# Kernel optimization log

Measured on AMD Instinct MI355X. Metric: run time of the kernel, lower is better.

## Reference

```python
import jax, jax.numpy as jnp
import numpy as np
from jax import lax

V_JOINTS = 25
N_SCALES = 13
C1 = 96
N_SEG = 50
EPS = 1e-5

# NTU RGB+D 25-joint skeleton edges (0-indexed)
_EDGES = [(0,1),(1,20),(2,20),(3,2),(4,20),(5,4),(6,5),(7,6),(8,20),(9,8),
          (10,9),(11,10),(12,0),(13,12),(14,13),(15,14),(16,0),(17,16),
          (18,17),(19,18),(21,22),(22,7),(23,24),(24,11)]


def _build_A_powers():
    # MS-G3D disentangled multi-scale adjacency: k-hop shells, D^-1/2 A D^-1/2 normalized
    A = np.zeros((V_JOINTS, V_JOINTS), dtype=np.float64)
    for i, j in _EDGES:
        A[i, j] = 1.0
        A[j, i] = 1.0
    I = np.eye(V_JOINTS)
    mats = []
    for k in range(N_SCALES):
        if k == 0:
            Ak = I.copy()
        else:
            Ak = (np.minimum(np.linalg.matrix_power(A + I, k), 1)
                  - np.minimum(np.linalg.matrix_power(A + I, k - 1), 1))
            Ak = Ak + I  # with_self=True
        d = Ak.sum(-1)
        Dinv = np.diag(d ** -0.5)
        mats.append(Dinv @ Ak @ Dinv)
    return np.concatenate(mats, axis=0).astype(np.float32)  # (13*25, 25)


def _segments(T, n_seg):
    # Segment boundaries exactly as the torch code: int(round(linspace(1, T, n_seg+1)))
    t_vec = [int(round(v)) for v in np.linspace(1, T, n_seg + 1)]
    lens = [t_vec[i + 1] - t_vec[i] for i in range(n_seg)]
    L = max(lens)
    idx = np.zeros((n_seg, L), dtype=np.int32)
    mask = np.zeros((n_seg, L), dtype=np.float32)
    for s in range(n_seg):
        start = t_vec[s] - 1
        for l in range(L):
            idx[s, l] = min(start + l, T - 2)
            mask[s, l] = 1.0 if l < lens[s] else 0.0
    sp_idx = np.array([t - 1 for t in t_vec[:-1]], dtype=np.int32)
    return idx, mask, sp_idx


def setup_inputs() -> dict:
    key = jax.random.key(0)
    ks = jax.random.split(key, 18)
    N, M, C, T, V = 4, 2, 3, 300, V_JOINTS
    num_classes = 60
    Cbn = M * C * V                       # 150
    Dlog = C1 + C1 * (C1 - 1) // 2        # 4656 (depth-2 logsig dims)
    Din = C1 + Dlog                       # 4752 (start pos + logsig)
    f = lambda k, s: jax.random.normal(k, s, dtype=jnp.float32)
    return {
        'x': f(ks[0], (N, M, C, T, V)),
        'bn_g': 1.0 + 0.1 * f(ks[1], (Cbn,)),
        'bn_b': 0.1 * f(ks[2], (Cbn,)),
        'bn_m': 0.1 * f(ks[3], (Cbn,)),
        'bn_v': jax.random.uniform(ks[4], (Cbn,), minval=0.5, maxval=1.5),
        'A_powers': jnp.asarray(_build_A_powers()),
        'A_res': jax.random.uniform(ks[5], (N_SCALES * V, V), minval=-1e-6, maxval=1e-6),
        'W_gcn': f(ks[6], (C1, N_SCALES * C)) / np.sqrt(N_SCALES * C),
        'b_gcn': 0.1 * f(ks[7], (C1,)),
        'bn2_g': 1.0 + 0.1 * f(ks[8], (C1,)),
        'bn2_b': 0.1 * f(ks[9], (C1,)),
        'bn2_m': 0.1 * f(ks[10], (C1,)),
        'bn2_v': jax.random.uniform(ks[11], (C1,), minval=0.5, maxval=1.5),
        'W_ih': f(ks[12], (4 * C1, Din)) / np.sqrt(Din),
        'W_hh': f(ks[13], (4 * C1, C1)) / np.sqrt(C1),
        'b_ih': 0.1 * f(ks[14], (4 * C1,)),
        'b_hh': 0.1 * f(ks[15], (4 * C1,)),
        'W_fc': f(ks[16], (num_classes, C1)) / np.sqrt(C1),
        'b_fc': 0.1 * f(ks[17], (num_classes,)),
    }


def reference(x, bn_g, bn_b, bn_m, bn_v, A_powers, A_res, W_gcn, b_gcn,
              bn2_g, bn2_b, bn2_m, bn2_v, W_ih, W_hh, b_ih, b_hh, W_fc, b_fc):
    N, M, C, T, V = x.shape
    NM = N * M
    # --- data_bn (inference BatchNorm1d over M*V*C channels) ---
    xb = x.transpose(0, 1, 4, 2, 3).reshape(N, M * V * C, T)
    xb = (xb - bn_m[:, None]) * (bn_g / jnp.sqrt(bn_v + EPS))[:, None] + bn_b[:, None]
    xg = xb.reshape(NM, V, C, T).transpose(0, 2, 3, 1)          # (NM, C, T, V)
    # --- MS_GCN: multi-scale disentangled graph conv ---
    A = A_powers + A_res                                        # (S*V, V)
    sup = jnp.einsum('vu,nctu->nctv', A, xg)                    # (NM, C, T, S*V)
    sup = sup.reshape(NM, C, T, N_SCALES, V).transpose(0, 3, 1, 2, 4)
    sup = sup.reshape(NM, N_SCALES * C, T, V)
    y = jnp.einsum('oc,nctv->notv', W_gcn, sup) + b_gcn[None, :, None, None]
    y = (y - bn2_m[None, :, None, None]) * (bn2_g / jnp.sqrt(bn2_v + EPS))[None, :, None, None] \
        + bn2_b[None, :, None, None]
    y = jax.nn.relu(y)                                          # (NM, C1, T, V)
    # --- LogSigRNN: per-joint temporal path, depth-2 log-signature per segment ---
    p = y.transpose(0, 3, 2, 1).reshape(NM * V, T, C1)          # (B, T, C1)
    idx, mask, sp_idx = _segments(T, N_SEG)
    dx = jnp.diff(p, axis=1)                                    # (B, T-1, C1)
    dseg = dx[:, idx] * mask[None, :, :, None]                  # (B, nseg, L, C1)
    pseg = jnp.cumsum(dseg, axis=2) - dseg                      # exclusive prefix within segment
    s1 = dseg.sum(axis=2)                                       # level-1: total increment
    Q = jnp.einsum('bslc,bsld->bscd', pseg, dseg)               # (B, nseg, C1, C1)
    levy = 0.5 * (Q - jnp.swapaxes(Q, -1, -2))                  # level-2 (Levy area)
    iu, ju = np.triu_indices(C1, 1)
    ls2 = levy[:, :, iu, ju]                                    # (B, nseg, 4560)
    start_pos = p[:, sp_idx, :]                                 # (B, nseg, C1)
    feat = jnp.concatenate([start_pos, s1, ls2], axis=-1)       # (B, nseg, 4752)
    # --- LSTM (torch gate order i,f,g,o) ---
    B = feat.shape[0]
    xw = jnp.einsum('btd,gd->btg', feat, W_ih) + (b_ih + b_hh)
    def step(carry, xt):
        h, c = carry
        g = xt + h @ W_hh.T
        i, fg, gg, o = jnp.split(g, 4, axis=-1)
        c = jax.nn.sigmoid(fg) * c + jax.nn.sigmoid(i) * jnp.tanh(gg)
        h = jax.nn.sigmoid(o) * jnp.tanh(c)
        return (h, c), h
    h0 = jnp.zeros((B, C1), feat.dtype)
    _, hs = lax.scan(step, (h0, h0), jnp.swapaxes(xw, 0, 1))
    hs = jnp.swapaxes(hs, 0, 1)                                 # (B, nseg, C1)
    out = hs.reshape(NM, V, N_SEG, C1).transpose(0, 3, 2, 1)    # (NM, C1, nseg, V)
    out = out.reshape(N, M, C1, -1).mean(axis=3).mean(axis=1)   # (N, C1)
    return out @ W_fc.T + b_fc
```

## Files before the change

### kernel.cpp

```cpp
#include <hip/hip_runtime.h>
#include <math.h>

#define KF 4752
#define KP 4768
#define KSTEPS 149
#define G4 384
#define NPAIR 4560
#define EPSBN 1e-5f
#define XWHALF 3840000

typedef float f32x4 __attribute__((ext_vector_type(4)));
typedef short s16x8 __attribute__((ext_vector_type(8)));

__device__ __forceinline__ unsigned short f2bf(float x){
  unsigned u = __float_as_uint(x);
  return (unsigned short)((u + 0x7fffu + ((u>>16)&1u)) >> 16);
}
__device__ __forceinline__ float bf2f(unsigned short h){
  return __uint_as_float(((unsigned)h)<<16);
}

__device__ __forceinline__ int seg_start(int s){ return (s<=24)? 6*s : 149 + 6*(s-25); }
__device__ __forceinline__ int seg_len(int s){ return (s==24)?5:6; }

#define NB_GEFF 1407
#define NB_BEFF 1200
#define NB_PAIR 18
#define NB_WSPL 7152

__global__ __launch_bounds__(256) void kPre(
    const float* bn_g,const float* bn_b,const float* bn_m,const float* bn_v,
    const float* Ap,const float* Ar,const float* Wg,const float* bg,
    const float* bn2_g,const float* bn2_b,const float* bn2_m,const float* bn2_v,
    const float* wih,
    float* geffT, float* beffT, int* pairs, unsigned short* whi, unsigned short* wlo)
{
  int bid = blockIdx.x, tid = threadIdx.x;
  if (bid < NB_GEFF){
    int idx = bid*256 + tid;
    if (idx >= 2*96*25*75) return;
    int cu = idx % 75; int rest = idx/75;
    int v = rest % 25; rest /= 25;
    int o = rest % 96; int m = rest / 96;
    int c = cu/25, u = cu%25;
    int ch = (m*25+u)*3 + c;
    float s1 = bn_g[ch] / sqrtf(bn_v[ch] + EPSBN);
    float s2 = bn2_g[o] / sqrtf(bn2_v[o] + EPSBN);
    float acc = 0.f;
    for (int k=0;k<13;k++){
      float a = Ap[(k*25+v)*25+u] + Ar[(k*25+v)*25+u];
      acc += Wg[o*39 + k*3 + c] * a;
    }
    geffT[((size_t)(m*75+cu))*2400 + v*96 + o] = acc * s1 * s2;
  } else if (bid < NB_GEFF + NB_BEFF){
    int wid  = ((bid-NB_GEFF)*256 + tid) >> 6;
    int lane = tid & 63;
    if (wid >= 2*96*25) return;
    int v = wid % 25; int rest = wid/25; int o = rest % 96; int m = rest/96;
    float acc = 0.f;
    #pragma unroll
    for (int it=0; it<16; ++it){
      int item = it*64 + lane;
      if (item < 975){
        int k = item / 75; int cu = item % 75; int c = cu/25, u = cu%25;
        int ch = (m*25+u)*3 + c;
        float s1 = bn_g[ch] / sqrtf(bn_v[ch] + EPSBN);
        float t1 = bn_b[ch] - bn_m[ch]*s1;
        float a  = Ap[(k*25+v)*25+u] + Ar[(k*25+v)*25+u];
        acc += Wg[o*39 + k*3 + c] * a * t1;
      }
    }
    #pragma unroll
    for (int off=32; off; off>>=1) acc += __shfl_down(acc, off);
    if (lane == 0){
      acc += bg[o];
      float s2 = bn2_g[o]/sqrtf(bn2_v[o]+EPSBN);
      beffT[m*2400 + v*96 + o] = s2*(acc - bn2_m[o]) + bn2_b[o];
    }
  } else if (bid < NB_GEFF + NB_BEFF + NB_PAIR){
    int k = (bid - NB_GEFF - NB_BEFF)*256 + tid;
    if (k >= NPAIR) return;
    int i=0, rem=k;
    while (rem >= 95 - i){ rem -= (95 - i); i++; }
    int j = i + 1 + rem;
    pairs[k] = (i<<7) | j;
  } else {
    int idx = (bid - NB_GEFF - NB_BEFF - NB_PAIR)*256 + tid;
    if (idx >= G4*KP) return;
    int g = idx / KP, k = idx % KP;
    float v = (k < KF) ? wih[(size_t)g*KF + k] : 0.f;
    unsigned short h = f2bf(v);
    whi[idx] = h;
    wlo[idx] = f2bf(v - bf2f(h));
  }
}

#define TTILE 10
__global__ __launch_bounds__(256) void kP(const float* x, const float* geffT, const float* beffT, float* p){
  int nm = blockIdx.y;
  int t0 = blockIdx.x * TTILE;
  int m  = nm % 2;
  __shared__ float xs[75*TTILE];
  int tid = threadIdx.x;
  for (int li = tid; li < 75*TTILE; li += 256){
    int u = li % 25; int rest = li/25; int tt = rest % TTILE; int c = rest / TTILE;
    xs[(c*25+u)*TTILE + tt] = x[(((size_t)nm*3 + c)*300 + (t0+tt))*25 + u];
  }
  __syncthreads();
  const float* gT = geffT + (size_t)m*75*2400;
  for (int ow = tid; ow < 2400; ow += 256){
    int o = ow % 96, v = ow / 96;
    float b = beffT[m*2400 + ow];
    float acc[TTILE];
    #pragma unroll
    for (int t=0;t<TTILE;t++) acc[t] = b;
    for (int cu=0; cu<75; cu++){
      float gv = gT[(size_t)cu*2400 + ow];
      #pragma unroll
      for (int t=0;t<TTILE;t++) acc[t] += gv * xs[cu*TTILE+t];
    }
    #pragma unroll
    for (int t=0;t<TTILE;t++)
      p[((size_t)(nm*25+v)*300 + t0+t)*96 + o] = fmaxf(acc[t], 0.f);
  }
}

__global__ __launch_bounds__(256) void kFeat(const float* p, const int* pairs,
                                             unsigned short* fhi, unsigned short* flo, int row0){
  int row = row0 + blockIdx.x;
  int b = row / 50, s = row % 50;
  int S = seg_start(s), len = seg_len(s);
  __shared__ float ps8[96][12];
  __shared__ float ds8[96][12];
  int tid = threadIdx.x;
  size_t base = (size_t)blockIdx.x * KP;
  if (tid < 96){
    int c = tid;
    float pv[7];
    #pragma unroll
    for (int l=0;l<7;l++) pv[l] = p[((size_t)b*300 + S + l)*96 + c];
    float run = 0.f;
    #pragma unroll
    for (int l=0;l<6;l++){
      float d = (l < len) ? (pv[l+1]-pv[l]) : 0.f;
      ps8[c][l] = run; ds8[c][l] = d; run += d;
    }
    ps8[c][6] = 0.f; ps8[c][7] = 0.f; ds8[c][6] = 0.f; ds8[c][7] = 0.f;
    unsigned short h0 = f2bf(pv[0]);
    fhi[base + c] = h0; flo[base + c] = f2bf(pv[0] - bf2f(h0));
    unsigned short h1 = f2bf(run);
    fhi[base + 96 + c] = h1; flo[base + 96 + c] = f2bf(run - bf2f(h1));
  } else if (tid < 112){
    int c = KF + (tid - 96);
    fhi[base + c] = 0; flo[base + c] = 0;
  }
  __syncthreads();
  for (int g8 = tid; g8 < NPAIR/8; g8 += 256){
    int k0 = g8*8;
    s16x8 vh, vl;
    int icur = -1;
    f32x4 pi0={0,0,0,0}, pi1={0,0,0,0}, di0={0,0,0,0}, di1={0,0,0,0};
    #pragma unroll
    for (int e=0;e<8;e++){
      int pr = pairs[k0+e]; int i = pr>>7, j = pr&127;
      if (i != icur){
        icur = i;
        pi0 = *(const f32x4*)&ps8[i][0]; pi1 = *(const f32x4*)&ps8[i][4];
        di0 = *(const f32x4*)&ds8[i][0]; di1 = *(const f32x4*)&ds8[i][4];
      }
      f32x4 pj0 = *(const f32x4*)&ps8[j][0], pj1 = *(const f32x4*)&ps8[j][4];
      f32x4 dj0 = *(const f32x4*)&ds8[j][0], dj1 = *(const f32x4*)&ds8[j][4];
      float q = pi0.x*dj0.x + pi0.y*dj0.y + pi0.z*dj0.z + pi0.w*dj0.w
              + pi1.x*dj1.x + pi1.y*dj1.y
              - pj0.x*di0.x - pj0.y*di0.y - pj0.z*di0.z - pj0.w*di0.w
              - pj1.x*di1.x - pj1.y*di1.y;
      q *= 0.5f;
      unsigned short h = f2bf(q);
      vh[e] = (short)h;
      vl[e] = (short)f2bf(q - bf2f(h));
    }
    *(s16x8*)(fhi + base + 192 + k0) = vh;
    *(s16x8*)(flo + base + 192 + k0) = vl;
  }
}

__device__ __forceinline__ void gload16(const void* g, void* l){
  __builtin_amdgcn_global_load_lds(
      (const __attribute__((address_space(1))) void*)g,
      (__attribute__((address_space(3))) void*)l, 16, 0, 0);
}

__global__ __launch_bounds__(256) void kGemm(
    const unsigned short* __restrict__ fhi, const unsigned short* __restrict__ flo,
    const unsigned short* __restrict__ whi, const unsigned short* __restrict__ wlo,
    float* __restrict__ xw, int chunkRow0, int nrows, int nmblk)
{
  __shared__ unsigned short lds[2][28672];
  int tid  = threadIdx.x;
  int lane = tid & 63, w = tid >> 6;
  int id = blockIdx.x;
  int col, zz, mblk;
  if (nmblk == 40){
    int xcd = id & 7, rank = id >> 3, s2 = rank >> 1;
    col = rank & 1;
    int pp = s2*8 + xcd;
    mblk = pp >> 1; zz = pp & 1;
  } else { col = id & 1; zz = (id >> 1) & 1; mblk = id >> 2; }
  int rowBase = mblk*256, colBase = col*192;
  int zbase = zz*75, zSteps = zz ? 74 : 75;

  int off[14];
  #pragma unroll
  for (int q=0;q<14;q++){
    int c = q*256 + tid;
    int rr = (q<4) ? c : (q<8) ? c-1024 : (q<11) ? c-2048 : c-2816;
    int rw = rr>>2, gl = rr&3;
    int gs = gl ^ ((rw>>1)&3);
    int grow = (q<8) ? (rowBase + rw) : (colBase + rw);
    off[q] = grow*KP + gs*8;
  }

  int wm = w & 1, wn = w >> 1;
  int gsel = lane >> 4, li = lane & 15;
  int aoff[8], boff[6];
  #pragma unroll
  for (int fm=0; fm<8; fm++){
    int r = wm*128 + fm*16 + li;
    aoff[fm] = r*32 + ((gsel ^ ((r>>1)&3))*8);
  }
  #pragma unroll
  for (int fn=0; fn<6; fn++){
    int r = wn*96 + fn*16 + li;
    boff[fn] = 16384 + r*32 + ((gsel ^ ((r>>1)&3))*8);
  }

  f32x4 acc[8][6];
  #pragma unroll
  for (int fm=0;fm<8;fm++)
    #pragma unroll
    for (int fn=0;fn<6;fn++) acc[fm][fn] = (f32x4){0.f,0.f,0.f,0.f};

#define STAGE(BUF, T) { \
    int ko = (zbase + (T))*32; \
    _Pragma("unroll") \
    for (int q=0;q<14;q++){ \
      const unsigned short* bp = (q<4)?fhi:(q<8)?flo:(q<11)?whi:wlo; \
      gload16(bp + (size_t)(off[q] + ko), &lds[BUF][q*2048 + w*512]); \
    } }

#define COMPUTE(BI) { \
    const unsigned short* L = lds[BI]; \
    s16x8 bh[6], bl[6]; \
    _Pragma("unroll") \
    for (int fn=0;fn<6;fn++){ \
      bh[fn] = *(const s16x8*)(L + boff[fn]); \
      bl[fn] = *(const s16x8*)(L + boff[fn] + 6144); \
    } \
    _Pragma("unroll") \
    for (int fm=0;fm<8;fm++){ \
      s16x8 ah = *(const s16x8*)(L + aoff[fm]); \
      s16x8 al = *(const s16x8*)(L + aoff[fm] + 8192); \
      _Pragma("unroll") \
      for (int fn=0;fn<6;fn++){ \
        acc[fm][fn] = __builtin_amdgcn_mfma_f32_16x16x32_bf16(ah, bh[fn], acc[fm][fn], 0,0,0); \
        acc[fm][fn] = __builtin_amdgcn_mfma_f32_16x16x32_bf16(ah, bl[fn], acc[fm][fn], 0,0,0); \
        acc[fm][fn] = __builtin_amdgcn_mfma_f32_16x16x32_bf16(al, bh[fn], acc[fm][fn], 0,0,0); \
      } \
    } }

  STAGE(0, 0);
  for (int t=0; t<zSteps-1; ++t){
    __builtin_amdgcn_s_barrier();
    STAGE((t+1)&1, t+1);
    asm volatile("s_waitcnt vmcnt(14)" ::: "memory");
    COMPUTE(t&1);
  }
  __builtin_amdgcn_s_barrier();
  asm volatile("s_waitcnt vmcnt(0)" ::: "memory");
  COMPUTE((zSteps-1)&1);

  int rl = (lane>>4)*4, cl = lane&15;
  float* outp = xw + (size_t)zz*XWHALF;
  #pragma unroll
  for (int fm=0;fm<8;fm++){
    #pragma unroll
    for (int fn=0;fn<6;fn++){
      int gr0 = rowBase + wm*128 + fm*16 + rl;
      int gc  = colBase + wn*96 + fn*16 + cl;
      f32x4 v = acc[fm][fn];
      #pragma unroll
      for (int r=0;r<4;r++){
        int gr = gr0 + r;
        if (gr < nrows)
          outp[(size_t)(chunkRow0 + gr)*G4 + gc] = v[r];
      }
    }
  }
#undef STAGE
#undef COMPUTE
}

__global__ __launch_bounds__(192) void kLstm(const float* xw, const float* whh,
                                             const float* bih, const float* bhh, float* hsum){
  int b = blockIdx.x;
  int t = threadIdx.x;
  int gA = t;
  int gB = t + 192;
  __shared__ __align__(16) float h_s[96];
  __shared__ float gbuf[384];
  float wA[96], wB[96];
  #pragma unroll
  for (int k=0;k<96;k++){ wA[k] = whh[(size_t)gA*96 + k]; wB[k] = whh[(size_t)gB*96 + k]; }
  float bA = bih[gA] + bhh[gA];
  float bB = bih[gB] + bhh[gB];
  float cval = 0.f, hacc = 0.f;
  if (t < 96) h_s[t] = 0.f;
  __syncthreads();
  const float* xr = xw + (size_t)b*50*G4;
  for (int st=0; st<50; st++){
    int o = st*G4;
    float aA = xr[o+gA] + xr[XWHALF+o+gA] + bA;
    float aB = xr[o+gB] + xr[XWHALF+o+gB] + bB;
    #pragma unroll
    for (int k=0;k<96;k+=4){
      float4 h4 = *(const float4*)&h_s[k];
      aA += wA[k]*h4.x + wA[k+1]*h4.y + wA[k+2]*h4.z + wA[k+3]*h4.w;
      aB += wB[k]*h4.x + wB[k+1]*h4.y + wB[k+2]*h4.z + wB[k+3]*h4.w;
    }
    gbuf[gA] = aA; gbuf[gB] = aB;
    __syncthreads();
    if (t < 96){
      float ig = gbuf[t], fg = gbuf[96+t], gg = gbuf[192+t], og = gbuf[288+t];
      float si = 1.f/(1.f+expf(-ig));
      float sf = 1.f/(1.f+expf(-fg));
      float so = 1.f/(1.f+expf(-og));
      cval = sf*cval + si*tanhf(gg);
      float h = so * tanhf(cval);
      h_s[t] = h;
      hacc += h;
    }
    __syncthreads();
  }
  if (t < 96) hsum[(size_t)b*96 + t] = hacc;
}

__global__ void kOut(const float* hsum, const float* wfc, const float* bfc, float* out){
  int n = blockIdx.x;
  __shared__ float pool[96];
  int tid = threadIdx.x;
  if (tid < 96){
    float a = 0.f;
    for (int mv=0; mv<50; mv++) a += hsum[((size_t)(n*50 + mv))*96 + tid];
    pool[tid] = a / 2500.f;
  }
  __syncthreads();
  if (tid < 60){
    float a = bfc[tid];
    for (int o=0;o<96;o++) a += pool[o]*wfc[tid*96+o];
    out[n*60+tid] = a;
  }
}

extern "C" void kernel_launch(void* const* d_in, const int* in_sizes, int n_in,
                              void* d_out, int out_size, void* d_ws, size_t ws_size,
                              hipStream_t stream){
  const float* x     = (const float*)d_in[0];
  const float* bn_g  = (const float*)d_in[1];
  const float* bn_b  = (const float*)d_in[2];
  const float* bn_m  = (const float*)d_in[3];
  const float* bn_v  = (const float*)d_in[4];
  const float* Ap    = (const float*)d_in[5];
  const float* Ar    = (const float*)d_in[6];
  const float* Wg    = (const float*)d_in[7];
  const float* bg    = (const float*)d_in[8];
  const float* bn2_g = (const float*)d_in[9];
  const float* bn2_b = (const float*)d_in[10];
  const float* bn2_m = (const float*)d_in[11];
  const float* bn2_v = (const float*)d_in[12];
  const float* wih   = (const float*)d_in[13];
  const float* whh   = (const float*)d_in[14];
  const float* bih   = (const float*)d_in[15];
  const float* bhh   = (const float*)d_in[16];
  const float* wfc   = (const float*)d_in[17];
  const float* bfc   = (const float*)d_in[18];
  float* out = (float*)d_out;

  float* ws    = (float*)d_ws;
  float* geffT = ws;
  float* beffT = geffT + 360000;
  int*   pairs = (int*)(beffT + 4800);
  float* pbuf  = beffT + 4800 + 4560;
  float* xw    = pbuf + 5760000;
  float* hsum  = xw + 2*(size_t)XWHALF;
  unsigned short* whiP = (unsigned short*)(hsum + 19200);
  unsigned short* wloP = whiP + (size_t)G4*KP;
  unsigned short* fhi  = wloP + (size_t)G4*KP;
  size_t fixedFloats = 360000u + 4800u + 4560u + 5760000u + 2u*(size_t)XWHALF + 19200u
                     + (size_t)G4*KP;
  long long availB = (long long)ws_size - (long long)(fixedFloats*4);
  long long perUnit = 256LL*KP*4;
  long long units = (availB > 0) ? availB/perUnit : 1;
  if (units < 1)  units = 1;
  if (units > 40) units = 40;
  int chunk = (int)units * 256;
  unsigned short* flo = fhi + (size_t)chunk*KP;

  kPre<<<NB_GEFF+NB_BEFF+NB_PAIR+NB_WSPL, 256, 0, stream>>>(
      bn_g, bn_b, bn_m, bn_v, Ap, Ar, Wg, bg, bn2_g, bn2_b, bn2_m, bn2_v,
      wih, geffT, beffT, pairs, whiP, wloP);
  kP<<<dim3(30, 8), 256, 0, stream>>>(x, geffT, beffT, pbuf);

  for (int r0 = 0; r0 < 10000; r0 += chunk){
    int nr = 10000 - r0; if (nr > chunk) nr = chunk;
    kFeat<<<nr, 256, 0, stream>>>(pbuf, pairs, fhi, flo, r0);
    int mblkc = (nr + 255)/256;
    kGemm<<<4*mblkc, 256, 0, stream>>>(fhi, flo, whiP, wloP, xw, r0, nr, mblkc);
  }

  kLstm<<<200, 192, 0, stream>>>(xw, whh, bih, bhh, hsum);
  kOut<<<4, 128, 0, stream>>>(hsum, wfc, bfc, out);
}
```

Baseline: 476.1 us.

## Shrink GEMM tiles with 4-way split-K and tile Levy-area computation in kFeat

The GEMM tile drops from 256 to 128 rows and split-K goes from 2 to 4 ways, giving 8 blocks per row-block and a smaller LDS footprint for more parallelism and occupancy. The LDS double buffer is replaced by a single buffer that waits on every k-step, so global loads no longer overlap compute. kFeat now computes the Levy-area pairs as 6x6 register tiles into a shared buffer instead of doing per-pair index lookups, which removes the pairs table. The LSTM input must now sum four partial xw buffers, and the workspace layout and chunk sizing change to match.

```diff
diff --git a/kernel.cpp b/kernel.cpp
--- a/kernel.cpp
+++ b/kernel.cpp
@@ -25,7 +25,6 @@
 
 #define NB_GEFF 1407
 #define NB_BEFF 1200
-#define NB_PAIR 18
 #define NB_WSPL 7152
 
 __global__ __launch_bounds__(256) void kPre(
@@ -33,7 +32,7 @@
     const float* Ap,const float* Ar,const float* Wg,const float* bg,
     const float* bn2_g,const float* bn2_b,const float* bn2_m,const float* bn2_v,
     const float* wih,
-    float* geffT, float* beffT, int* pairs, unsigned short* whi, unsigned short* wlo)
+    float* geffT, float* beffT, unsigned short* whi, unsigned short* wlo)
 {
   int bid = blockIdx.x, tid = threadIdx.x;
   if (bid < NB_GEFF){
@@ -77,15 +76,8 @@
       float s2 = bn2_g[o]/sqrtf(bn2_v[o]+EPSBN);
       beffT[m*2400 + v*96 + o] = s2*(acc - bn2_m[o]) + bn2_b[o];
     }
-  } else if (bid < NB_GEFF + NB_BEFF + NB_PAIR){
-    int k = (bid - NB_GEFF - NB_BEFF)*256 + tid;
-    if (k >= NPAIR) return;
-    int i=0, rem=k;
-    while (rem >= 95 - i){ rem -= (95 - i); i++; }
-    int j = i + 1 + rem;
-    pairs[k] = (i<<7) | j;
   } else {
-    int idx = (bid - NB_GEFF - NB_BEFF - NB_PAIR)*256 + tid;
+    int idx = (bid - NB_GEFF - NB_BEFF)*256 + tid;
     if (idx >= G4*KP) return;
     int g = idx / KP, k = idx % KP;
     float v = (k < KF) ? wih[(size_t)g*KF + k] : 0.f;
@@ -125,13 +117,14 @@
   }
 }
 
-__global__ __launch_bounds__(256) void kFeat(const float* p, const int* pairs,
+__global__ __launch_bounds__(256) void kFeat(const float* p,
                                              unsigned short* fhi, unsigned short* flo, int row0){
   int row = row0 + blockIdx.x;
   int b = row / 50, s = row % 50;
   int S = seg_start(s), len = seg_len(s);
-  __shared__ float ps8[96][12];
-  __shared__ float ds8[96][12];
+  __shared__ float psL[6][96];
+  __shared__ float dsL[6][96];
+  __shared__ float qbuf[NPAIR];
   int tid = threadIdx.x;
   size_t base = (size_t)blockIdx.x * KP;
   if (tid < 96){
@@ -143,9 +136,8 @@
     #pragma unroll
     for (int l=0;l<6;l++){
       float d = (l < len) ? (pv[l+1]-pv[l]) : 0.f;
-      ps8[c][l] = run; ds8[c][l] = d; run += d;
-    }
-    ps8[c][6] = 0.f; ps8[c][7] = 0.f; ds8[c][6] = 0.f; ds8[c][7] = 0.f;
+      psL[l][c] = run; dsL[l][c] = d; run += d;
+    }
     unsigned short h0 = f2bf(pv[0]);
     fhi[base + c] = h0; flo[base + c] = f2bf(pv[0] - bf2f(h0));
     unsigned short h1 = f2bf(run);
@@ -155,32 +147,53 @@
     fhi[base + c] = 0; flo[base + c] = 0;
   }
   __syncthreads();
+  int ti = tid >> 4, tj = tid & 15;
+  if (ti <= tj){
+    int i0 = ti*6, j0 = tj*6;
+    float q[6][6];
+    #pragma unroll
+    for (int a=0;a<6;a++)
+      #pragma unroll
+      for (int e=0;e<6;e++) q[a][e] = 0.f;
+    #pragma unroll
+    for (int l=0;l<6;l++){
+      float pi[6], di[6], pj[6], dj[6];
+      #pragma unroll
+      for (int a=0;a<6;a++){
+        pi[a] = psL[l][i0+a]; di[a] = dsL[l][i0+a];
+        pj[a] = psL[l][j0+a]; dj[a] = dsL[l][j0+a];
+      }
+      #pragma unroll
+      for (int a=0;a<6;a++)
+        #pragma unroll
+        for (int e=0;e<6;e++)
+          q[a][e] += pi[a]*dj[e] - pj[e]*di[a];
+    }
+    #pragma unroll
+    for (int a=0;a<6;a++){
+      int i = i0 + a;
+      int kb = i*95 - (i*(i-1))/2 - i - 1;
+      #pragma unroll
+      for (int e=0;e<6;e++){
+        int j = j0 + e;
+        if (j > i) qbuf[kb + j] = 0.5f*q[a][e];
+      }
+    }
+  }
+  __syncthreads();
   for (int g8 = tid; g8 < NPAIR/8; g8 += 256){
-    int k0 = g8*8;
+    f32x4 q0 = *(const f32x4*)&qbuf[g8*8];
+    f32x4 q1 = *(const f32x4*)&qbuf[g8*8+4];
+    float qa[8] = {q0.x,q0.y,q0.z,q0.w,q1.x,q1.y,q1.z,q1.w};
     s16x8 vh, vl;
-    int icur = -1;
-    f32x4 pi0={0,0,0,0}, pi1={0,0,0,0}, di0={0,0,0,0}, di1={0,0,0,0};
     #pragma unroll
     for (int e=0;e<8;e++){
-      int pr = pairs[k0+e]; int i = pr>>7, j = pr&127;
-      if (i != icur){
-        icur = i;
-        pi0 = *(const f32x4*)&ps8[i][0]; pi1 = *(const f32x4*)&ps8[i][4];
-        di0 = *(const f32x4*)&ds8[i][0]; di1 = *(const f32x4*)&ds8[i][4];
-      }
-      f32x4 pj0 = *(const f32x4*)&ps8[j][0], pj1 = *(const f32x4*)&ps8[j][4];
-      f32x4 dj0 = *(const f32x4*)&ds8[j][0], dj1 = *(const f32x4*)&ds8[j][4];
-      float q = pi0.x*dj0.x + pi0.y*dj0.y + pi0.z*dj0.z + pi0.w*dj0.w
-              + pi1.x*dj1.x + pi1.y*dj1.y
-              - pj0.x*di0.x - pj0.y*di0.y - pj0.z*di0.z - pj0.w*di0.w
-              - pj1.x*di1.x - pj1.y*di1.y;
-      q *= 0.5f;
-      unsigned short h = f2bf(q);
+      unsigned short h = f2bf(qa[e]);
       vh[e] = (short)h;
-      vl[e] = (short)f2bf(q - bf2f(h));
-    }
-    *(s16x8*)(fhi + base + 192 + k0) = vh;
-    *(s16x8*)(flo + base + 192 + k0) = vl;
+      vl[e] = (short)f2bf(qa[e] - bf2f(h));
+    }
+    *(s16x8*)(fhi + base + 192 + g8*8) = vh;
+    *(s16x8*)(flo + base + 192 + g8*8) = vl;
   }
 }
 
@@ -193,99 +206,86 @@
 __global__ __launch_bounds__(256) void kGemm(
     const unsigned short* __restrict__ fhi, const unsigned short* __restrict__ flo,
     const unsigned short* __restrict__ whi, const unsigned short* __restrict__ wlo,
-    float* __restrict__ xw, int chunkRow0, int nrows, int nmblk)
+    float* __restrict__ xw, int chunkRow0, int nrows)
 {
-  __shared__ unsigned short lds[2][28672];
+  __shared__ unsigned short lds[20480];
   int tid  = threadIdx.x;
   int lane = tid & 63, w = tid >> 6;
   int id = blockIdx.x;
-  int col, zz, mblk;
-  if (nmblk == 40){
-    int xcd = id & 7, rank = id >> 3, s2 = rank >> 1;
-    col = rank & 1;
-    int pp = s2*8 + xcd;
-    mblk = pp >> 1; zz = pp & 1;
-  } else { col = id & 1; zz = (id >> 1) & 1; mblk = id >> 2; }
-  int rowBase = mblk*256, colBase = col*192;
-  int zbase = zz*75, zSteps = zz ? 74 : 75;
-
-  int off[14];
-  #pragma unroll
-  for (int q=0;q<14;q++){
-    int c = q*256 + tid;
-    int rr = (q<4) ? c : (q<8) ? c-1024 : (q<11) ? c-2048 : c-2816;
+  int col = id & 1, zz = (id >> 1) & 3, mblk = id >> 3;
+  int rowBase = mblk*128, colBase = col*192;
+  int zbase = (zz==0) ? 0 : (38 + 37*(zz-1));
+  int zSteps = (zz==0) ? 38 : 37;
+
+  const unsigned short* gptr[10];
+  int ldsOff[10];
+  #pragma unroll
+  for (int q=0;q<10;q++){
+    int c = (w*10 + q)*64 + lane;
+    const unsigned short* bp; int rr;
+    if (c < 512)        { rr = c;        bp = fhi + (size_t)(rowBase + (rr>>2))*KP; }
+    else if (c < 1024)  { rr = c-512;    bp = flo + (size_t)(rowBase + (rr>>2))*KP; }
+    else if (c < 1792)  { rr = c-1024;   bp = whi + (size_t)(colBase + (rr>>2))*KP; }
+    else                { rr = c-1792;   bp = wlo + (size_t)(colBase + (rr>>2))*KP; }
     int rw = rr>>2, gl = rr&3;
     int gs = gl ^ ((rw>>1)&3);
-    int grow = (q<8) ? (rowBase + rw) : (colBase + rw);
-    off[q] = grow*KP + gs*8;
+    gptr[q]  = bp + gs*8;
+    ldsOff[q] = (w*10 + q)*512;
   }
 
   int wm = w & 1, wn = w >> 1;
   int gsel = lane >> 4, li = lane & 15;
-  int aoff[8], boff[6];
-  #pragma unroll
-  for (int fm=0; fm<8; fm++){
-    int r = wm*128 + fm*16 + li;
+  int aoff[4], boff[6];
+  #pragma unroll
+  for (int fm=0; fm<4; fm++){
+    int r = wm*64 + fm*16 + li;
     aoff[fm] = r*32 + ((gsel ^ ((r>>1)&3))*8);
   }
   #pragma unroll
   for (int fn=0; fn<6; fn++){
     int r = wn*96 + fn*16 + li;
-    boff[fn] = 16384 + r*32 + ((gsel ^ ((r>>1)&3))*8);
-  }
-
-  f32x4 acc[8][6];
-  #pragma unroll
-  for (int fm=0;fm<8;fm++)
+    boff[fn] = 8192 + r*32 + ((gsel ^ ((r>>1)&3))*8);
+  }
+
+  f32x4 acc[4][6];
+  #pragma unroll
+  for (int fm=0;fm<4;fm++)
     #pragma unroll
     for (int fn=0;fn<6;fn++) acc[fm][fn] = (f32x4){0.f,0.f,0.f,0.f};
 
-#define STAGE(BUF, T) { \
-    int ko = (zbase + (T))*32; \
-    _Pragma("unroll") \
-    for (int q=0;q<14;q++){ \
-      const unsigned short* bp = (q<4)?fhi:(q<8)?flo:(q<11)?whi:wlo; \
-      gload16(bp + (size_t)(off[q] + ko), &lds[BUF][q*2048 + w*512]); \
-    } }
-
-#define COMPUTE(BI) { \
-    const unsigned short* L = lds[BI]; \
-    s16x8 bh[6], bl[6]; \
-    _Pragma("unroll") \
-    for (int fn=0;fn<6;fn++){ \
-      bh[fn] = *(const s16x8*)(L + boff[fn]); \
-      bl[fn] = *(const s16x8*)(L + boff[fn] + 6144); \
-    } \
-    _Pragma("unroll") \
-    for (int fm=0;fm<8;fm++){ \
-      s16x8 ah = *(const s16x8*)(L + aoff[fm]); \
-      s16x8 al = *(const s16x8*)(L + aoff[fm] + 8192); \
-      _Pragma("unroll") \
-      for (int fn=0;fn<6;fn++){ \
-        acc[fm][fn] = __builtin_amdgcn_mfma_f32_16x16x32_bf16(ah, bh[fn], acc[fm][fn], 0,0,0); \
-        acc[fm][fn] = __builtin_amdgcn_mfma_f32_16x16x32_bf16(ah, bl[fn], acc[fm][fn], 0,0,0); \
-        acc[fm][fn] = __builtin_amdgcn_mfma_f32_16x16x32_bf16(al, bh[fn], acc[fm][fn], 0,0,0); \
-      } \
-    } }
-
-  STAGE(0, 0);
-  for (int t=0; t<zSteps-1; ++t){
+  for (int t=0; t<zSteps; ++t){
+    size_t ko = (size_t)(zbase + t)*32;
+    #pragma unroll
+    for (int q=0;q<10;q++) gload16(gptr[q] + ko, &lds[ldsOff[q]]);
+    asm volatile("s_waitcnt vmcnt(0)" ::: "memory");
     __builtin_amdgcn_s_barrier();
-    STAGE((t+1)&1, t+1);
-    asm volatile("s_waitcnt vmcnt(14)" ::: "memory");
-    COMPUTE(t&1);
-  }
-  __builtin_amdgcn_s_barrier();
-  asm volatile("s_waitcnt vmcnt(0)" ::: "memory");
-  COMPUTE((zSteps-1)&1);
+    s16x8 bh[6], bl[6];
+    #pragma unroll
+    for (int fn=0;fn<6;fn++){
+      bh[fn] = *(const s16x8*)(lds + boff[fn]);
+      bl[fn] = *(const s16x8*)(lds + boff[fn] + 6144);
+    }
+    #pragma unroll
+    for (int fm=0;fm<4;fm++){
+      s16x8 ah = *(const s16x8*)(lds + aoff[fm]);
+      s16x8 al = *(const s16x8*)(lds + aoff[fm] + 4096);
+      #pragma unroll
+      for (int fn=0;fn<6;fn++){
+        acc[fm][fn] = __builtin_amdgcn_mfma_f32_16x16x32_bf16(ah, bh[fn], acc[fm][fn], 0,0,0);
+        acc[fm][fn] = __builtin_amdgcn_mfma_f32_16x16x32_bf16(ah, bl[fn], acc[fm][fn], 0,0,0);
+        acc[fm][fn] = __builtin_amdgcn_mfma_f32_16x16x32_bf16(al, bh[fn], acc[fm][fn], 0,0,0);
+      }
+    }
+    __builtin_amdgcn_s_barrier();
+  }
 
   int rl = (lane>>4)*4, cl = lane&15;
   float* outp = xw + (size_t)zz*XWHALF;
   #pragma unroll
-  for (int fm=0;fm<8;fm++){
+  for (int fm=0;fm<4;fm++){
     #pragma unroll
     for (int fn=0;fn<6;fn++){
-      int gr0 = rowBase + wm*128 + fm*16 + rl;
+      int gr0 = rowBase + wm*64 + fm*16 + rl;
       int gc  = colBase + wn*96 + fn*16 + cl;
       f32x4 v = acc[fm][fn];
       #pragma unroll
@@ -296,8 +296,6 @@
       }
     }
   }
-#undef STAGE
-#undef COMPUTE
 }
 
 __global__ __launch_bounds__(192) void kLstm(const float* xw, const float* whh,
@@ -319,8 +317,10 @@
   const float* xr = xw + (size_t)b*50*G4;
   for (int st=0; st<50; st++){
     int o = st*G4;
-    float aA = xr[o+gA] + xr[XWHALF+o+gA] + bA;
-    float aB = xr[o+gB] + xr[XWHALF+o+gB] + bB;
+    float aA = xr[o+gA] + xr[XWHALF+o+gA] + xr[2*(size_t)XWHALF+o+gA]
+             + xr[3*(size_t)XWHALF+o+gA] + bA;
+    float aB = xr[o+gB] + xr[XWHALF+o+gB] + xr[2*(size_t)XWHALF+o+gB]
+             + xr[3*(size_t)XWHALF+o+gB] + bB;
     #pragma unroll
     for (int k=0;k<96;k+=4){
       float4 h4 = *(const float4*)&h_s[k];
@@ -388,33 +388,32 @@
   float* ws    = (float*)d_ws;
   float* geffT = ws;
   float* beffT = geffT + 360000;
-  int*   pairs = (int*)(beffT + 4800);
-  float* pbuf  = beffT + 4800 + 4560;
+  float* pbuf  = beffT + 4800;
   float* xw    = pbuf + 5760000;
-  float* hsum  = xw + 2*(size_t)XWHALF;
+  float* hsum  = xw + 4*(size_t)XWHALF;
   unsigned short* whiP = (unsigned short*)(hsum + 19200);
   unsigned short* wloP = whiP + (size_t)G4*KP;
   unsigned short* fhi  = wloP + (size_t)G4*KP;
-  size_t fixedFloats = 360000u + 4800u + 4560u + 5760000u + 2u*(size_t)XWHALF + 19200u
+  size_t fixedFloats = 360000u + 4800u + 5760000u + 4u*(size_t)XWHALF + 19200u
                      + (size_t)G4*KP;
   long long availB = (long long)ws_size - (long long)(fixedFloats*4);
-  long long perUnit = 256LL*KP*4;
+  long long perUnit = 128LL*KP*4;
   long long units = (availB > 0) ? availB/perUnit : 1;
   if (units < 1)  units = 1;
-  if (units > 40) units = 40;
-  int chunk = (int)units * 256;
+  if (units > 79) units = 79;
+  int chunk = (int)units * 128;
   unsigned short* flo = fhi + (size_t)chunk*KP;
 
-  kPre<<<NB_GEFF+NB_BEFF+NB_PAIR+NB_WSPL, 256, 0, stream>>>(
+  kPre<<<NB_GEFF+NB_BEFF+NB_WSPL, 256, 0, stream>>>(
       bn_g, bn_b, bn_m, bn_v, Ap, Ar, Wg, bg, bn2_g, bn2_b, bn2_m, bn2_v,
-      wih, geffT, beffT, pairs, whiP, wloP);
+      wih, geffT, beffT, whiP, wloP);
   kP<<<dim3(30, 8), 256, 0, stream>>>(x, geffT, beffT, pbuf);
 
   for (int r0 = 0; r0 < 10000; r0 += chunk){
     int nr = 10000 - r0; if (nr > chunk) nr = chunk;
-    kFeat<<<nr, 256, 0, stream>>>(pbuf, pairs, fhi, flo, r0);
-    int mblkc = (nr + 255)/256;
-    kGemm<<<4*mblkc, 256, 0, stream>>>(fhi, flo, whiP, wloP, xw, r0, nr, mblkc);
+    kFeat<<<nr, 256, 0, stream>>>(pbuf, fhi, flo, r0);
+    int mblkc = (nr + 127)/128;
+    kGemm<<<8*mblkc, 256, 0, stream>>>(fhi, flo, whiP, wloP, xw, r0, nr);
   }
 
   kLstm<<<200, 192, 0, stream>>>(xw, whh, bih, bhh, hsum);
```

Result: no change. 468.8 us (median of 2 runs) (-1.5%).
